# Performance work log

Measured on AMD Instinct MI355X. Metric: run time of the kernel, lower is better.

## Reference

```python
import jax, jax.numpy as jnp
import numpy as np

B, T, E, H, HD = 4, 1500, 1280, 20, 64
SCALING = HD ** -0.5


def setup_inputs() -> dict:
    key = jax.random.key(0)
    ks = jax.random.split(key, 8)
    s = 0.02
    return {
        "hidden_states": jax.random.normal(ks[0], (B, 1, T, E), jnp.float32),
        "attention_mask": jnp.zeros((B, 1, T, T), jnp.float32),
        "Wq": jax.random.normal(ks[1], (H, HD, E), jnp.float32) * s,
        "bq": jax.random.normal(ks[2], (H, HD), jnp.float32) * s,
        "Wk": jax.random.normal(ks[3], (H, HD, E), jnp.float32) * s,
        "Wv": jax.random.normal(ks[4], (H, HD, E), jnp.float32) * s,
        "bv": jax.random.normal(ks[5], (H, HD), jnp.float32) * s,
        "Wo": jax.random.normal(ks[6], (E, E), jnp.float32) * s,
        "bo": jax.random.normal(ks[7], (E,), jnp.float32) * s,
    }


def reference(hidden_states, attention_mask, Wq, bq, Wk, Wv, bv, Wo, bo):
    # hidden_states: [B, 1, T, E] (NHWC with H=1, as in the torch module)
    b, _, t, e = hidden_states.shape
    x = hidden_states[:, 0]  # [B, T, E]
    # Per-head 1x1 Conv2d projections == batched linear over stacked head weights.
    # Scaling is folded into q (the module bakes it into q_proj weights/bias).
    q = (jnp.einsum("bte,hde->bhtd", x, Wq) + bq[None, :, None, :]) * SCALING
    k = jnp.einsum("bse,hde->bhsd", x, Wk)
    v = jnp.einsum("bse,hde->bhsd", x, Wv) + bv[None, :, None, :]
    # attention_mask broadcasts over the head dim (module adds it per head as [B,1,T,S])
    scores = jnp.einsum("bhtd,bhsd->bhts", q, k) + attention_mask  # [B,H,T,S]
    attn = jax.nn.softmax(scores, axis=-1)
    out = jnp.einsum("bhts,bhsd->bhtd", attn, v)  # [B,H,T,HD]
    out = out.transpose(0, 2, 1, 3).reshape(b, t, e)  # concat heads on channel dim
    final = jnp.einsum("bte,fe->btf", out, Wo) + bo  # 1x1 Conv2d out_proj
    return final[:, None, :, :]  # [B,1,T,E]
```

## Files before the change

### kernel.cpp

```cpp
#include <hip/hip_runtime.h>

#define T_LEN 1500
#define TP    1536
#define EDIM  1280
#define NH    20
#define HD    64
#define KDIM  1280
#define NT    20

#define LOG2E 1.4426950408889634f

#define OFF_X    ((size_t)0)
#define OFF_AO   ((size_t)0)
#define OFF_W    ((size_t)7700480)
#define OFF_WO   ((size_t)12615680)
#define OFF_Q    ((size_t)14254080)
#define OFF_K    ((size_t)22118400)
#define OFF_VT   ((size_t)29982720)

typedef float  f32x4  __attribute__((ext_vector_type(4)));
typedef float  f32x16 __attribute__((ext_vector_type(16)));
typedef short  s16x8  __attribute__((ext_vector_type(8)));
typedef __bf16 bf16x8 __attribute__((ext_vector_type(8)));
typedef unsigned short u16;
typedef unsigned int   u32;
typedef unsigned int u32x4 __attribute__((ext_vector_type(4)));

__device__ __forceinline__ f32x4 mfma_bf16(s16x8 a, s16x8 b, f32x4 c) {
  return __builtin_amdgcn_mfma_f32_16x16x32_bf16(
      __builtin_bit_cast(bf16x8, a), __builtin_bit_cast(bf16x8, b), c, 0, 0, 0);
}

__device__ __forceinline__ f32x16 mfma32(s16x8 a, s16x8 b, f32x16 c) {
  return __builtin_amdgcn_mfma_f32_32x32x16_bf16(
      __builtin_bit_cast(bf16x8, a), __builtin_bit_cast(bf16x8, b), c, 0, 0, 0);
}

__device__ __forceinline__ u16 f2bf(float f) {
  union { float f; unsigned int u; } a; a.f = f;
  return (u16)((a.u + 0x7fffu + ((a.u >> 16) & 1u)) >> 16);
}

__device__ __forceinline__ float fexp2(float x) {
  return __builtin_amdgcn_exp2f(x);
}

__device__ __forceinline__ void gl_lds16(const u16* g, u16* l) {
  __builtin_amdgcn_global_load_lds(
      (const __attribute__((address_space(1))) unsigned int*)(const void*)g,
      (__attribute__((address_space(3))) unsigned int*)(void*)l, 16, 0, 0);
}


__global__ __launch_bounds__(256) void prep_kernel(
    const float* __restrict__ x, const float* __restrict__ wq,
    const float* __restrict__ wk, const float* __restrict__ wv,
    const float* __restrict__ wo, const float* __restrict__ mask,
    u16* __restrict__ ws, u32* __restrict__ nzflags) {
  const int S0 = 1925120;
  const int S1 = 1228800;
  const int S2 = 409600;
  const int P1 = 46080;
  const int S3 = 2250000;
  const int TOT = S0 + S1 + S2 + 3 * P1 + S3;
  for (int v = blockIdx.x * 256 + threadIdx.x; v < TOT; v += gridDim.x * 256) {
    if (v < S0) {
      int i = v * 4;
      int m = i / EDIM, e = i - m * EDIM;
      int ep = (e & ~63) | (((((e >> 3) & 7) ^ (m & 7))) << 3) | (e & 7);
      ushort4 o;
      if (m < 6000) {
        float4 f = *(const float4*)(x + i);
        o = make_ushort4(f2bf(f.x), f2bf(f.y), f2bf(f.z), f2bf(f.w));
      } else {
        o = make_ushort4(0, 0, 0, 0);
      }
      *(ushort4*)(ws + OFF_X + (size_t)m * EDIM + ep) = o;
    } else if (v < S0 + S1) {
      int j = (v - S0) * 4;
      int n = j / EDIM, e = j - n * EDIM;
      const float* s = (n < 1280) ? wq + (size_t)n * EDIM + e
                     : (n < 2560) ? wk + (size_t)(n - 1280) * EDIM + e
                                  : wv + (size_t)(n - 2560) * EDIM + e;
      float4 f = *(const float4*)s;
      int ep = (e & ~63) | (((((e >> 3) & 7) ^ (n & 7))) << 3) | (e & 7);
      *(ushort4*)(ws + OFF_W + (size_t)n * EDIM + ep) =
          make_ushort4(f2bf(f.x), f2bf(f.y), f2bf(f.z), f2bf(f.w));
    } else if (v < S0 + S1 + S2) {
      int j = (v - S0 - S1) * 4;
      int n = j / EDIM, e = j - n * EDIM;
      float4 f = *(const float4*)(wo + j);
      int ep = (e & ~63) | (((((e >> 3) & 7) ^ (n & 7))) << 3) | (e & 7);
      *(ushort4*)(ws + OFF_WO + (size_t)n * EDIM + ep) =
          make_ushort4(f2bf(f.x), f2bf(f.y), f2bf(f.z), f2bf(f.w));
    } else if (v < S0 + S1 + S2 + 3 * P1) {
      int p = v - (S0 + S1 + S2);
      ushort4 z = make_ushort4(0, 0, 0, 0);
      if (p < P1) {
        int p4 = p * 4; int bh = p4 / 2304; int rem = p4 - bh * 2304;
        int tt = rem >> 6, d = rem & 63;
        *(ushort4*)(ws + OFF_Q + ((size_t)(bh * TP + 1500 + tt)) * HD + d) = z;
      } else if (p < 2 * P1) {
        int p4 = (p - P1) * 4; int bh = p4 / 2304; int rem = p4 - bh * 2304;
        int tt = rem >> 6, d = rem & 63;
        *(ushort4*)(ws + OFF_K + ((size_t)(bh * TP + 1500 + tt)) * HD + d) = z;
      } else {
        int p4 = (p - 2 * P1) * 4; int bh = p4 / 2304; int rem = p4 - bh * 2304;
        int d = rem / 36, ss = rem - d * 36;
        int t = 1500 + ss;
        int tphys = (t & ~63) | (((((t >> 3) & 7) ^ (d & 7))) << 3) | (t & 7);
        *(ushort4*)(ws + OFF_VT + ((size_t)(bh * HD + d)) * TP + tphys) = z;
      }
    } else {
      int p = v - (S0 + S1 + S2 + 3 * P1);
      int i4 = p * 4;
      int bb = i4 / 2250000;
      int rem = i4 - bb * 2250000;
      int q = rem / 1500;
      int s = rem - q * 1500;
      float4 f = *(const float4*)(mask + (size_t)bb * 2250000 + rem);
      if (f.x != 0.f || f.y != 0.f || f.z != 0.f || f.w != 0.f)
        atomicOr(&nzflags[(bb * 12 + (q >> 7)) * 24 + (s >> 6)], 1u);
    }
  }
}

__device__ __forceinline__ void gemm_mainloop256(
    const u16* __restrict__ A, const u16* __restrict__ B,
    int mt, int nt, u16* lds, f32x4 acc[4][4]) {
  const int tid = threadIdx.x;
  const int lane = tid & 63, wid = tid >> 6;
  const int lg = lane >> 4, lr = lane & 15;
  const int wr = wid >> 1, wn = wid & 1;

  const u16* aB = A + (size_t)(mt * 256) * KDIM;
  const u16* bB = B + (size_t)(nt * 128) * KDIM;
  size_t aOff[4], bOff[2];
  #pragma unroll
  for (int l = 0; l < 4; ++l) {
    int gid = l * 512 + tid;
    aOff[l] = (size_t)(gid >> 3) * KDIM + (gid & 7) * 8;
  }
  #pragma unroll
  for (int l = 0; l < 2; ++l) {
    int gid = l * 512 + tid;
    bOff[l] = (size_t)(gid >> 3) * KDIM + (gid & 7) * 8;
  }
  const int ldsOff = tid * 8;
  int arow[4], brow[4];
  #pragma unroll
  for (int i = 0; i < 4; ++i) arow[i] = (wr * 64 + i * 16 + lr) * 64;
  #pragma unroll
  for (int j = 0; j < 4; ++j) brow[j] = (wn * 64 + j * 16 + lr) * 64;
  const int gsw0 = ((lg) ^ (lr & 7)) * 8;
  const int gsw1 = ((4 + lg) ^ (lr & 7)) * 8;

  #pragma unroll
  for (int t = 0; t < 2; ++t) {
    u16* dA = lds + t * 24576;
    u16* dB = dA + 16384;
    gl_lds16(aB + aOff[0] + t * 64, dA + ldsOff);
    gl_lds16(aB + aOff[1] + t * 64, dA + ldsOff + 4096);
    gl_lds16(bB + bOff[0] + t * 64, dB + ldsOff);
    gl_lds16(aB + aOff[2] + t * 64, dA + ldsOff + 8192);
    gl_lds16(aB + aOff[3] + t * 64, dA + ldsOff + 12288);
    gl_lds16(bB + bOff[1] + t * 64, dB + ldsOff + 4096);
  }
  asm volatile("s_waitcnt vmcnt(6)" ::: "memory");
  __builtin_amdgcn_s_barrier();
  __builtin_amdgcn_sched_barrier(0);
  s16x8 ca[4], cb[4];
  #pragma unroll
  for (int i = 0; i < 4; ++i) ca[i] = *(const s16x8*)(lds + arow[i] + gsw0);
  #pragma unroll
  for (int j = 0; j < 4; ++j) cb[j] = *(const s16x8*)(lds + 16384 + brow[j] + gsw0);

  int s = 0;
  #pragma unroll 1
  for (int kt = 0; kt < NT; ++kt) {
    u16* cA = lds + s * 24576;
    u16* cB = cA + 16384;
    int ssl = s + 2; if (ssl >= 3) ssl -= 3;
    u16* sA = lds + ssl * 24576;
    u16* sB = sA + 16384;
    const bool doStage = (kt + 2 < NT);
    if (doStage) {
      gl_lds16(aB + aOff[0] + (kt + 2) * 64, sA + ldsOff);
      gl_lds16(aB + aOff[1] + (kt + 2) * 64, sA + ldsOff + 4096);
      gl_lds16(bB + bOff[0] + (kt + 2) * 64, sB + ldsOff);
    }
    s16x8 na[4], nb[4];
    #pragma unroll
    for (int i = 0; i < 4; ++i) na[i] = *(const s16x8*)(cA + arow[i] + gsw1);
    #pragma unroll
    for (int j = 0; j < 4; ++j) nb[j] = *(const s16x8*)(cB + brow[j] + gsw1);
    __builtin_amdgcn_s_setprio(1);
    #pragma unroll
    for (int i = 0; i < 4; ++i)
      #pragma unroll
      for (int j = 0; j < 4; ++j)
        acc[i][j] = mfma_bf16(ca[i], cb[j], acc[i][j]);
    __builtin_amdgcn_s_setprio(0);
    if (doStage) {
      gl_lds16(aB + aOff[2] + (kt + 2) * 64, sA + ldsOff + 8192);
      gl_lds16(aB + aOff[3] + (kt + 2) * 64, sA + ldsOff + 12288);
      gl_lds16(bB + bOff[1] + (kt + 2) * 64, sB + ldsOff + 4096);
    }
    if (kt < NT - 1) {
      asm volatile("s_waitcnt lgkmcnt(0)" ::: "memory");
      if (kt < NT - 2) asm volatile("s_waitcnt vmcnt(6)" ::: "memory");
      else             asm volatile("s_waitcnt vmcnt(0)" ::: "memory");
      __builtin_amdgcn_s_barrier();
      __builtin_amdgcn_sched_barrier(0);
      int sn = s + 1; if (sn >= 3) sn = 0;
      const u16* nA = lds + sn * 24576;
      const u16* nB2 = nA + 16384;
      #pragma unroll
      for (int i = 0; i < 4; ++i) ca[i] = *(const s16x8*)(nA + arow[i] + gsw0);
      #pragma unroll
      for (int j = 0; j < 4; ++j) cb[j] = *(const s16x8*)(nB2 + brow[j] + gsw0);
    }
    __builtin_amdgcn_s_setprio(1);
    #pragma unroll
    for (int i = 0; i < 4; ++i)
      #pragma unroll
      for (int j = 0; j < 4; ++j)
        acc[i][j] = mfma_bf16(na[i], nb[j], acc[i][j]);
    __builtin_amdgcn_s_setprio(0);
    s = s + 1; if (s >= 3) s = 0;
  }
}

__global__ __launch_bounds__(512) void gemm_qkv_kernel(
    const u16* __restrict__ X, const u16* __restrict__ W,
    const float* __restrict__ bq, const float* __restrict__ bv,
    u16* __restrict__ Qw, u16* __restrict__ Kw, u16* __restrict__ Vtw) {
  __shared__ __align__(16) u16 lds[3 * 24576];
  const int bid = blockIdx.x;
  const int xcd = bid & 7, idx = bid >> 3;
  const int mt = xcd * 3 + idx % 3;
  const int nt = idx / 3;
  f32x4 acc[4][4] = {};
  gemm_mainloop256(X, W, mt, nt, lds, acc);
  const int tid = threadIdx.x;
  const int lane = tid & 63, wid = tid >> 6;
  const int lg = lane >> 4, lr = lane & 15;
  const int wr = wid >> 1, wn = wid & 1;
  #pragma unroll
  for (int i = 0; i < 4; ++i) {
    #pragma unroll
    for (int r = 0; r < 4; ++r) {
      int mm = mt * 256 + wr * 64 + i * 16 + lg * 4 + r;
      if (mm >= 6000) continue;
      int bt = mm / 1500, tt = mm - bt * 1500;
      #pragma unroll
      for (int j = 0; j < 4; ++j) {
        int n = nt * 128 + wn * 64 + j * 16 + lr;
        float v = acc[i][j][r];
        if (n < 1280) {
          int hh = n >> 6, d = n & 63;
          Qw[((size_t)(bt * NH + hh) * TP + tt) * HD + d] =
              f2bf((v + bq[n]) * (0.125f * LOG2E));
        } else if (n < 2560) {
          int nn = n - 1280, hh = nn >> 6, d = nn & 63;
          int dp = ((((d >> 3) ^ (tt & 7))) << 3) | (d & 7);
          Kw[((size_t)(bt * NH + hh) * TP + tt) * HD + dp] = f2bf(v);
        } else {
          int nn = n - 2560, hh = nn >> 6, d = nn & 63;
          int tphys = (tt & ~63) | (((((tt >> 3) & 7) ^ (d & 7))) << 3) | (tt & 7);
          Vtw[((size_t)(bt * NH + hh) * HD + d) * TP + tphys] = f2bf(v + bv[nn]);
        }
      }
    }
  }
}

__global__ __launch_bounds__(256) void attn_kernel(
    const u16* __restrict__ Qw, const u16* __restrict__ Kw,
    const u16* __restrict__ Vtw, const float* __restrict__ mask,
    const u32* __restrict__ nzflags, u16* __restrict__ AO) {
  __shared__ __align__(16) u16 Kb[2][64 * 64];
  __shared__ __align__(16) u16 Vb[2][64 * 64];
  const int bid = blockIdx.x;
  const int qt = bid / 80;
  const int bhid = bid % 80;
  const int bb = bhid / NH, hh = bhid % NH;
  const int tid = threadIdx.x;
  const int w = tid >> 6;
  const int lane = tid & 63;
  const int lq = lane & 31;
  const int hi = lane >> 5;
  const int q0 = qt * 128 + w * 32;
  const int qrow = q0 + lq;
  const int qm = qrow < (T_LEN - 1) ? qrow : (T_LEN - 1);
  const u16* Qp = Qw + (size_t)bhid * TP * HD;
  const u16* Kp = Kw + (size_t)bhid * TP * HD;
  const u16* Vp = Vtw + (size_t)bhid * HD * TP;
  const float* mp = mask + (size_t)bb * T_LEN * T_LEN + (size_t)qm * T_LEN;
  const u32* nzp = nzflags + (bb * 12 + qt) * 24;

  s16x8 qf[4];
  #pragma unroll
  for (int c = 0; c < 4; ++c)
    qf[c] = *(const s16x8*)(Qp + (size_t)qrow * HD + c * 16 + hi * 8);

  f32x16 O0 = {}, O1 = {};
  float m = -3e38f, l = 0.f;

  {
    gl_lds16(Kp + tid * 8,                 Kb[0] + tid * 8);
    gl_lds16(Kp + 2048 + tid * 8,          Kb[0] + 2048 + tid * 8);
    int r = tid >> 3, g = tid & 7;
    gl_lds16(Vp + (size_t)r * TP + g * 8,          Vb[0] + tid * 8);
    gl_lds16(Vp + (size_t)(r + 32) * TP + g * 8,   Vb[0] + 2048 + tid * 8);
  }
  __syncthreads();

  int buf = 0;
  #pragma unroll 1
  for (int st = 0; st < 24; ++st) {
    const int s0 = st * 64;
    if (st < 23) {
      const int sn = s0 + 64;
      gl_lds16(Kp + (size_t)sn * HD + tid * 8,        Kb[buf ^ 1] + tid * 8);
      gl_lds16(Kp + (size_t)sn * HD + 2048 + tid * 8, Kb[buf ^ 1] + 2048 + tid * 8);
      int r = tid >> 3, g = tid & 7;
      gl_lds16(Vp + (size_t)r * TP + sn + g * 8,        Vb[buf ^ 1] + tid * 8);
      gl_lds16(Vp + (size_t)(r + 32) * TP + sn + g * 8, Vb[buf ^ 1] + 2048 + tid * 8);
    }
    const bool has_mask = nzp[st] != 0u;
    const u16* kb = Kb[buf];
    f32x16 S0a = {}, S1a = {};
    #pragma unroll
    for (int c = 0; c < 4; ++c) {
      int gc = 2 * c + hi;
      int gs = (gc ^ (lq & 7)) << 3;
      s16x8 k0 = *(const s16x8*)(kb + lq * 64 + gs);
      s16x8 k1 = *(const s16x8*)(kb + (32 + lq) * 64 + gs);
      S0a = mfma32(k0, qf[c], S0a);
      S1a = mfma32(k1, qf[c], S1a);
    }
    float p[32];
    #pragma unroll
    for (int r = 0; r < 16; ++r) { p[r] = S0a[r]; p[16 + r] = S1a[r]; }
    if (has_mask) {
      f32x4 mk[2][4];
      #pragma unroll
      for (int sh = 0; sh < 2; ++sh)
        #pragma unroll
        for (int g = 0; g < 4; ++g) {
          int sb = s0 + sh * 32 + 8 * g + 4 * hi;
          if (sb > T_LEN - 4) sb = T_LEN - 4;
          mk[sh][g] = *(const f32x4*)(mp + sb);
        }
      #pragma unroll
      for (int r = 0; r < 16; ++r) {
        p[r]      = fmaf(mk[0][r >> 2][r & 3], LOG2E, p[r]);
        p[16 + r] = fmaf(mk[1][r >> 2][r & 3], LOG2E, p[16 + r]);
      }
    }
    if (st == 23) {
      if (hi) { p[12] = p[13] = p[14] = p[15] = -1e30f; }
      #pragma unroll
      for (int r = 16; r < 32; ++r) p[r] = -1e30f;
    }
    float t1[16];
    #pragma unroll
    for (int r = 0; r < 16; ++r) t1[r] = fmaxf(p[r], p[r + 16]);
    #pragma unroll
    for (int r = 0; r < 8; ++r) t1[r] = fmaxf(t1[r], t1[r + 8]);
    float mx = fmaxf(fmaxf(fmaxf(t1[0], t1[1]), fmaxf(t1[2], t1[3])),
                     fmaxf(fmaxf(t1[4], t1[5]), fmaxf(t1[6], t1[7])));
    mx = fmaxf(mx, __shfl_xor(mx, 32));
    if (!__all(mx <= m + 8.f)) {
      float mn = fmaxf(m, mx);
      float sc = fexp2(m - mn);
      O0 *= sc; O1 *= sc; l *= sc;
      m = mn;
    }
    #pragma unroll
    for (int r = 0; r < 32; ++r) p[r] = fexp2(p[r] - m);
    float s1[16];
    #pragma unroll
    for (int r = 0; r < 16; ++r) s1[r] = p[r] + p[r + 16];
    #pragma unroll
    for (int r = 0; r < 8; ++r) s1[r] += s1[r + 8];
    #pragma unroll
    for (int r = 0; r < 4; ++r) s1[r] += s1[r + 4];
    float rs = (s1[0] + s1[1]) + (s1[2] + s1[3]);
    rs += __shfl_xor(rs, 32);
    l += rs;
    const u16* vb = Vb[buf];
    #pragma unroll
    for (int sh = 0; sh < 2; ++sh) {
      u32 pk[8];
      #pragma unroll
      for (int j = 0; j < 8; ++j)
        asm("v_cvt_pk_bf16_f32 %0, %1, %2"
            : "=v"(pk[j]) : "v"(p[sh * 16 + 2 * j]), "v"(p[sh * 16 + 2 * j + 1]));
      asm("v_permlane32_swap_b32 %0, %1" : "+v"(pk[0]), "+v"(pk[2]));
      asm("v_permlane32_swap_b32 %0, %1" : "+v"(pk[1]), "+v"(pk[3]));
      asm("v_permlane32_swap_b32 %0, %1" : "+v"(pk[4]), "+v"(pk[6]));
      asm("v_permlane32_swap_b32 %0, %1" : "+v"(pk[5]), "+v"(pk[7]));
      u32x4 ta = {pk[0], pk[1], pk[2], pk[3]};
      u32x4 tb = {pk[4], pk[5], pk[6], pk[7]};
      s16x8 pfa = __builtin_bit_cast(s16x8, ta);
      s16x8 pfb = __builtin_bit_cast(s16x8, tb);
      int ga = sh * 4 + hi, gb = sh * 4 + 2 + hi;
      {
        int d = lq;
        s16x8 va = *(const s16x8*)(vb + d * 64 + ((ga ^ (d & 7)) << 3));
        s16x8 vc = *(const s16x8*)(vb + d * 64 + ((gb ^ (d & 7)) << 3));
        O0 = mfma32(va, pfa, O0);
        O0 = mfma32(vc, pfb, O0);
      }
      {
        int d = 32 + lq;
        s16x8 va = *(const s16x8*)(vb + d * 64 + ((ga ^ (d & 7)) << 3));
        s16x8 vc = *(const s16x8*)(vb + d * 64 + ((gb ^ (d & 7)) << 3));
        O1 = mfma32(va, pfa, O1);
        O1 = mfma32(vc, pfb, O1);
      }
    }
    __syncthreads();
    buf ^= 1;
  }

  if (qrow < T_LEN) {
    float inv = 1.f / l;
    int arow = bb * T_LEN + qrow;
    int key = arow & 7;
    size_t base = (size_t)arow * EDIM + hh * 64;
    #pragma unroll
    for (int g = 0; g < 4; ++g) {
      ushort4 o0, o1;
      o0.x = f2bf(O0[4 * g + 0] * inv); o0.y = f2bf(O0[4 * g + 1] * inv);
      o0.z = f2bf(O0[4 * g + 2] * inv); o0.w = f2bf(O0[4 * g + 3] * inv);
      o1.x = f2bf(O1[4 * g + 0] * inv); o1.y = f2bf(O1[4 * g + 1] * inv);
      o1.z = f2bf(O1[4 * g + 2] * inv); o1.w = f2bf(O1[4 * g + 3] * inv);
      *(ushort4*)(AO + base + ((g ^ key) << 3) + 4 * hi)       = o0;
      *(ushort4*)(AO + base + (((4 + g) ^ key) << 3) + 4 * hi) = o1;
    }
  }
}

__global__ __launch_bounds__(512) void gemm_out_kernel(
    const u16* __restrict__ AOb, const u16* __restrict__ Wob,
    const float* __restrict__ bo, float* __restrict__ out) {
  __shared__ __align__(16) u16 lds[3 * 24576];
  const int bid = blockIdx.x;
  const int xcd = bid & 7, idx = bid >> 3;
  const int mt = xcd * 3 + idx % 3;
  const int nt = idx / 3;
  f32x4 acc[4][4] = {};
  gemm_mainloop256(AOb, Wob, mt, nt, lds, acc);
  const int tid = threadIdx.x;
  const int lane = tid & 63, wid = tid >> 6;
  const int lg = lane >> 4, lr = lane & 15;
  const int wr = wid >> 1, wn = wid & 1;
  #pragma unroll
  for (int i = 0; i < 4; ++i) {
    #pragma unroll
    for (int r = 0; r < 4; ++r) {
      int mm = mt * 256 + wr * 64 + i * 16 + lg * 4 + r;
      if (mm >= 6000) continue;
      #pragma unroll
      for (int j = 0; j < 4; ++j) {
        int n = nt * 128 + wn * 64 + j * 16 + lr;
        out[(size_t)mm * EDIM + n] = acc[i][j][r] + bo[n];
      }
    }
  }
}

extern "C" void kernel_launch(void* const* d_in, const int* in_sizes, int n_in,
                              void* d_out, int out_size, void* d_ws, size_t ws_size,
                              hipStream_t stream) {
  const float* x    = (const float*)d_in[0];
  const float* mask = (const float*)d_in[1];
  const float* wq   = (const float*)d_in[2];
  const float* bq   = (const float*)d_in[3];
  const float* wk   = (const float*)d_in[4];
  const float* wv   = (const float*)d_in[5];
  const float* bv   = (const float*)d_in[6];
  const float* wo   = (const float*)d_in[7];
  const float* bo   = (const float*)d_in[8];
  float* out = (float*)d_out;
  u16* ws = (u16*)d_ws;
  u32* nzflags = (u32*)d_out;

  hipMemsetAsync(nzflags, 0, 1152 * sizeof(u32), stream);
  prep_kernel<<<2048, 256, 0, stream>>>(x, wq, wk, wv, wo, mask, ws, nzflags);
  gemm_qkv_kernel<<<720, 512, 0, stream>>>(
      ws + OFF_X, ws + OFF_W, bq, bv, ws + OFF_Q, ws + OFF_K, ws + OFF_VT);
  attn_kernel<<<960, 256, 0, stream>>>(
      ws + OFF_Q, ws + OFF_K, ws + OFF_VT, mask, nzflags, ws + OFF_AO);
  gemm_out_kernel<<<240, 512, 0, stream>>>(
      ws + OFF_AO, ws + OFF_WO, bo, out);
}
```

Baseline: 240.4 us.

## Halve GEMM K-tile to 32 with new 4-way swizzle and smaller LDS stages

The shared GEMM mainloop now uses a K-tile of 32 instead of 64, running 40 iterations with one MFMA batch and one barrier each instead of two batches per tile. The pre-swizzled bf16 layout of X, the weights and the attention output is changed to match, with a 4-way XOR on 32-element groups. LDS per block drops from 3x48KB to 3x24KB, which may allow more blocks per CU or reduce LDS pressure. The cost is twice as many barriers and waits per K, and less MFMA work available to hide global-to-LDS latency.

After: 240.9 us. No clear change (+0.2%).

```diff
diff --git a/kernel.cpp b/kernel.cpp
--- a/kernel.cpp
+++ b/kernel.cpp
@@ -6,7 +6,7 @@
 #define NH    20
 #define HD    64
 #define KDIM  1280
-#define NT    20
+#define NT    40
 
 #define LOG2E 1.4426950408889634f
 
@@ -51,6 +51,7 @@
       (__attribute__((address_space(3))) unsigned int*)(void*)l, 16, 0, 0);
 }
 
+__device__ __forceinline__ int perm4(int r) { return (r + (r >> 1)) & 3; }
 
 __global__ __launch_bounds__(256) void prep_kernel(
     const float* __restrict__ x, const float* __restrict__ wq,
@@ -67,7 +68,7 @@
     if (v < S0) {
       int i = v * 4;
       int m = i / EDIM, e = i - m * EDIM;
-      int ep = (e & ~63) | (((((e >> 3) & 7) ^ (m & 7))) << 3) | (e & 7);
+      int ep = (e & ~31) | (((((e >> 3) & 3) ^ perm4(m))) << 3) | (e & 7);
       ushort4 o;
       if (m < 6000) {
         float4 f = *(const float4*)(x + i);
@@ -83,14 +84,14 @@
                      : (n < 2560) ? wk + (size_t)(n - 1280) * EDIM + e
                                   : wv + (size_t)(n - 2560) * EDIM + e;
       float4 f = *(const float4*)s;
-      int ep = (e & ~63) | (((((e >> 3) & 7) ^ (n & 7))) << 3) | (e & 7);
+      int ep = (e & ~31) | (((((e >> 3) & 3) ^ perm4(n))) << 3) | (e & 7);
       *(ushort4*)(ws + OFF_W + (size_t)n * EDIM + ep) =
           make_ushort4(f2bf(f.x), f2bf(f.y), f2bf(f.z), f2bf(f.w));
     } else if (v < S0 + S1 + S2) {
       int j = (v - S0 - S1) * 4;
       int n = j / EDIM, e = j - n * EDIM;
       float4 f = *(const float4*)(wo + j);
-      int ep = (e & ~63) | (((((e >> 3) & 7) ^ (n & 7))) << 3) | (e & 7);
+      int ep = (e & ~31) | (((((e >> 3) & 3) ^ perm4(n))) << 3) | (e & 7);
       *(ushort4*)(ws + OFF_WO + (size_t)n * EDIM + ep) =
           make_ushort4(f2bf(f.x), f2bf(f.y), f2bf(f.z), f2bf(f.w));
     } else if (v < S0 + S1 + S2 + 3 * P1) {
@@ -135,99 +136,73 @@
 
   const u16* aB = A + (size_t)(mt * 256) * KDIM;
   const u16* bB = B + (size_t)(nt * 128) * KDIM;
-  size_t aOff[4], bOff[2];
-  #pragma unroll
-  for (int l = 0; l < 4; ++l) {
-    int gid = l * 512 + tid;
-    aOff[l] = (size_t)(gid >> 3) * KDIM + (gid & 7) * 8;
-  }
+  size_t aOff[2];
   #pragma unroll
   for (int l = 0; l < 2; ++l) {
     int gid = l * 512 + tid;
-    bOff[l] = (size_t)(gid >> 3) * KDIM + (gid & 7) * 8;
-  }
-  const int ldsOff = tid * 8;
-  int arow[4], brow[4];
-  #pragma unroll
-  for (int i = 0; i < 4; ++i) arow[i] = (wr * 64 + i * 16 + lr) * 64;
-  #pragma unroll
-  for (int j = 0; j < 4; ++j) brow[j] = (wn * 64 + j * 16 + lr) * 64;
-  const int gsw0 = ((lg) ^ (lr & 7)) * 8;
-  const int gsw1 = ((4 + lg) ^ (lr & 7)) * 8;
+    aOff[l] = (size_t)(gid >> 2) * KDIM + (gid & 3) * 8;
+  }
+  const size_t bOff = (size_t)(tid >> 2) * KDIM + (tid & 3) * 8;
+  const int ldsA = tid * 8;
+  const int ldsB = 8192 + tid * 8;
+  int ard[4], brd[4];
+  #pragma unroll
+  for (int i = 0; i < 4; ++i) {
+    int rho = wr * 64 + i * 16 + lr;
+    ard[i] = rho * 32 + ((lg ^ perm4(rho)) << 3);
+  }
+  #pragma unroll
+  for (int j = 0; j < 4; ++j) {
+    int beta = wn * 64 + j * 16 + lr;
+    brd[j] = 8192 + beta * 32 + ((lg ^ perm4(beta)) << 3);
+  }
 
   #pragma unroll
   for (int t = 0; t < 2; ++t) {
-    u16* dA = lds + t * 24576;
-    u16* dB = dA + 16384;
-    gl_lds16(aB + aOff[0] + t * 64, dA + ldsOff);
-    gl_lds16(aB + aOff[1] + t * 64, dA + ldsOff + 4096);
-    gl_lds16(bB + bOff[0] + t * 64, dB + ldsOff);
-    gl_lds16(aB + aOff[2] + t * 64, dA + ldsOff + 8192);
-    gl_lds16(aB + aOff[3] + t * 64, dA + ldsOff + 12288);
-    gl_lds16(bB + bOff[1] + t * 64, dB + ldsOff + 4096);
-  }
-  asm volatile("s_waitcnt vmcnt(6)" ::: "memory");
+    u16* sl = lds + t * 12288;
+    gl_lds16(aB + aOff[0] + t * 32, sl + ldsA);
+    gl_lds16(aB + aOff[1] + t * 32, sl + ldsA + 4096);
+    gl_lds16(bB + bOff + t * 32,    sl + ldsB);
+  }
+  asm volatile("s_waitcnt vmcnt(3)" ::: "memory");
   __builtin_amdgcn_s_barrier();
   __builtin_amdgcn_sched_barrier(0);
-  s16x8 ca[4], cb[4];
-  #pragma unroll
-  for (int i = 0; i < 4; ++i) ca[i] = *(const s16x8*)(lds + arow[i] + gsw0);
-  #pragma unroll
-  for (int j = 0; j < 4; ++j) cb[j] = *(const s16x8*)(lds + 16384 + brow[j] + gsw0);
-
-  int s = 0;
+  s16x8 fa[4], fb[4];
+  #pragma unroll
+  for (int i = 0; i < 4; ++i) fa[i] = *(const s16x8*)(lds + ard[i]);
+  #pragma unroll
+  for (int j = 0; j < 4; ++j) fb[j] = *(const s16x8*)(lds + brd[j]);
+
+  int s2 = 2, s1 = 1;
   #pragma unroll 1
   for (int kt = 0; kt < NT; ++kt) {
-    u16* cA = lds + s * 24576;
-    u16* cB = cA + 16384;
-    int ssl = s + 2; if (ssl >= 3) ssl -= 3;
-    u16* sA = lds + ssl * 24576;
-    u16* sB = sA + 16384;
-    const bool doStage = (kt + 2 < NT);
-    if (doStage) {
-      gl_lds16(aB + aOff[0] + (kt + 2) * 64, sA + ldsOff);
-      gl_lds16(aB + aOff[1] + (kt + 2) * 64, sA + ldsOff + 4096);
-      gl_lds16(bB + bOff[0] + (kt + 2) * 64, sB + ldsOff);
-    }
-    s16x8 na[4], nb[4];
-    #pragma unroll
-    for (int i = 0; i < 4; ++i) na[i] = *(const s16x8*)(cA + arow[i] + gsw1);
-    #pragma unroll
-    for (int j = 0; j < 4; ++j) nb[j] = *(const s16x8*)(cB + brow[j] + gsw1);
+    if (kt + 2 < NT) {
+      u16* sl = lds + s2 * 12288;
+      gl_lds16(aB + aOff[0] + (kt + 2) * 32, sl + ldsA);
+      gl_lds16(aB + aOff[1] + (kt + 2) * 32, sl + ldsA + 4096);
+      gl_lds16(bB + bOff + (kt + 2) * 32,    sl + ldsB);
+    }
     __builtin_amdgcn_s_setprio(1);
     #pragma unroll
     for (int i = 0; i < 4; ++i)
       #pragma unroll
       for (int j = 0; j < 4; ++j)
-        acc[i][j] = mfma_bf16(ca[i], cb[j], acc[i][j]);
+        acc[i][j] = mfma_bf16(fa[i], fb[j], acc[i][j]);
     __builtin_amdgcn_s_setprio(0);
-    if (doStage) {
-      gl_lds16(aB + aOff[2] + (kt + 2) * 64, sA + ldsOff + 8192);
-      gl_lds16(aB + aOff[3] + (kt + 2) * 64, sA + ldsOff + 12288);
-      gl_lds16(bB + bOff[1] + (kt + 2) * 64, sB + ldsOff + 4096);
-    }
     if (kt < NT - 1) {
       asm volatile("s_waitcnt lgkmcnt(0)" ::: "memory");
-      if (kt < NT - 2) asm volatile("s_waitcnt vmcnt(6)" ::: "memory");
+      if (kt < NT - 2) asm volatile("s_waitcnt vmcnt(3)" ::: "memory");
       else             asm volatile("s_waitcnt vmcnt(0)" ::: "memory");
       __builtin_amdgcn_s_barrier();
       __builtin_amdgcn_sched_barrier(0);
-      int sn = s + 1; if (sn >= 3) sn = 0;
-      const u16* nA = lds + sn * 24576;
-      const u16* nB2 = nA + 16384;
-      #pragma unroll
-      for (int i = 0; i < 4; ++i) ca[i] = *(const s16x8*)(nA + arow[i] + gsw0);
-      #pragma unroll
-      for (int j = 0; j < 4; ++j) cb[j] = *(const s16x8*)(nB2 + brow[j] + gsw0);
-    }
-    __builtin_amdgcn_s_setprio(1);
-    #pragma unroll
-    for (int i = 0; i < 4; ++i)
-      #pragma unroll
-      for (int j = 0; j < 4; ++j)
-        acc[i][j] = mfma_bf16(na[i], nb[j], acc[i][j]);
-    __builtin_amdgcn_s_setprio(0);
-    s = s + 1; if (s >= 3) s = 0;
+      const u16* ns = lds + s1 * 12288;
+      #pragma unroll
+      for (int i = 0; i < 4; ++i) fa[i] = *(const s16x8*)(ns + ard[i]);
+      #pragma unroll
+      for (int j = 0; j < 4; ++j) fb[j] = *(const s16x8*)(ns + brd[j]);
+    }
+    s2 = s2 + 1; if (s2 >= 3) s2 = 0;
+    s1 = s1 + 1; if (s1 >= 3) s1 = 0;
   }
 }
 
@@ -235,7 +210,7 @@
     const u16* __restrict__ X, const u16* __restrict__ W,
     const float* __restrict__ bq, const float* __restrict__ bv,
     u16* __restrict__ Qw, u16* __restrict__ Kw, u16* __restrict__ Vtw) {
-  __shared__ __align__(16) u16 lds[3 * 24576];
+  __shared__ __align__(16) u16 lds[3 * 12288];
   const int bid = blockIdx.x;
   const int xcd = bid & 7, idx = bid >> 3;
   const int mt = xcd * 3 + idx % 3;
@@ -429,7 +404,7 @@
   if (qrow < T_LEN) {
     float inv = 1.f / l;
     int arow = bb * T_LEN + qrow;
-    int key = arow & 7;
+    int pa = perm4(arow);
     size_t base = (size_t)arow * EDIM + hh * 64;
     #pragma unroll
     for (int g = 0; g < 4; ++g) {
@@ -438,8 +413,8 @@
       o0.z = f2bf(O0[4 * g + 2] * inv); o0.w = f2bf(O0[4 * g + 3] * inv);
       o1.x = f2bf(O1[4 * g + 0] * inv); o1.y = f2bf(O1[4 * g + 1] * inv);
       o1.z = f2bf(O1[4 * g + 2] * inv); o1.w = f2bf(O1[4 * g + 3] * inv);
-      *(ushort4*)(AO + base + ((g ^ key) << 3) + 4 * hi)       = o0;
-      *(ushort4*)(AO + base + (((4 + g) ^ key) << 3) + 4 * hi) = o1;
+      *(ushort4*)(AO + base + ((g ^ pa) << 3) + 4 * hi)       = o0;
+      *(ushort4*)(AO + base + 32 + ((g ^ pa) << 3) + 4 * hi)  = o1;
     }
   }
 }
@@ -447,7 +422,7 @@
 __global__ __launch_bounds__(512) void gemm_out_kernel(
     const u16* __restrict__ AOb, const u16* __restrict__ Wob,
     const float* __restrict__ bo, float* __restrict__ out) {
-  __shared__ __align__(16) u16 lds[3 * 24576];
+  __shared__ __align__(16) u16 lds[3 * 12288];
   const int bid = blockIdx.x;
   const int xcd = bid & 7, idx = bid >> 3;
   const int mt = xcd * 3 + idx % 3;
```
